# Kernel tuning notes

Hardware: AMD Instinct MI355X
Metric: run time of the kernel (lower is better)

## Reference

```python
import jax, jax.numpy as jnp
import numpy as np

EMBED = 1024
HEADS = 16
HEAD_DIM = EMBED // HEADS
MASKED_BIAS = -10000.0


def setup_inputs() -> dict:
    key = jax.random.key(0)
    k1, k2, k3 = jax.random.split(key, 3)
    hidden_states = jax.random.normal(k1, (4, 2048, EMBED), dtype=jnp.float32)
    c_attn_w = jax.random.normal(k2, (EMBED, 3 * EMBED), dtype=jnp.float32) * 0.02
    c_attn_b = jnp.zeros((3 * EMBED,), dtype=jnp.float32)
    c_proj_w = jax.random.normal(k3, (EMBED, EMBED), dtype=jnp.float32) * 0.02
    c_proj_b = jnp.zeros((EMBED,), dtype=jnp.float32)
    return {
        "hidden_states": hidden_states,
        "c_attn_w": c_attn_w,
        "c_attn_b": c_attn_b,
        "c_proj_w": c_proj_w,
        "c_proj_b": c_proj_b,
    }


def reference(hidden_states, c_attn_w, c_attn_b, c_proj_w, c_proj_b):
    B, S, E = hidden_states.shape
    # QKV projection (Conv1D == x @ W + b)
    qkv = hidden_states @ c_attn_w + c_attn_b  # [B,S,3E]
    q, k, v = jnp.split(qkv, 3, axis=-1)
    def split_heads(t):
        return t.reshape(B, S, HEADS, HEAD_DIM).transpose(0, 2, 1, 3)  # [B,H,S,D]
    q, k, v = split_heads(q), split_heads(k), split_heads(v)
    # scaled attention scores
    scores = jnp.einsum("bhqd,bhkd->bhqk", q, k) / jnp.float32(HEAD_DIM) ** 0.5
    causal = jnp.tril(jnp.ones((S, S), dtype=bool))
    scores = jnp.where(causal[None, None], scores, jnp.float32(MASKED_BIAS))
    attn_weights = jax.nn.softmax(scores, axis=-1)
    attn_out = jnp.einsum("bhqk,bhkd->bhqd", attn_weights, v)
    attn_out = attn_out.transpose(0, 2, 1, 3).reshape(B, S, E)
    out = attn_out @ c_proj_w + c_proj_b
    return out
```

## Files before the change

kernel.cpp:

```cpp
#include <hip/hip_runtime.h>
#include <hip/hip_bf16.h>

#define EMB 1024
#define SEQ 2048
#define ATT_SCALE 0.18033688011112042f

typedef __bf16 bf16x8 __attribute__((ext_vector_type(8)));
typedef float f32x4 __attribute__((ext_vector_type(4)));
typedef float f32x16 __attribute__((ext_vector_type(16)));

__device__ __forceinline__ unsigned short f2bf(float f) {
    union { float f; unsigned int u; } v; v.f = f;
    unsigned int r = (v.u + 0x7FFFu + ((v.u >> 16) & 1u)) >> 16;
    return (unsigned short)r;
}

__device__ __forceinline__ void async_load16(const void* g, void* l) {
    __builtin_amdgcn_global_load_lds(
        (const __attribute__((address_space(1))) unsigned int*)g,
        (__attribute__((address_space(3))) unsigned int*)l, 16, 0, 0);
}

__global__ void cvt_bf16(const float4* __restrict__ in, ushort4* __restrict__ out, int n4) {
    int i = blockIdx.x * blockDim.x + threadIdx.x;
    int stride = gridDim.x * blockDim.x;
    for (; i < n4; i += stride) {
        float4 v = in[i];
        ushort4 o;
        o.x = f2bf(v.x); o.y = f2bf(v.y); o.z = f2bf(v.z); o.w = f2bf(v.w);
        out[i] = o;
    }
}

__global__ void transpose_cvt(const float* __restrict__ in, unsigned short* __restrict__ out,
                              int R, int C) {
    __shared__ float tile[32][33];
    int bx = blockIdx.x * 32;
    int by = blockIdx.y * 32;
    int tx = threadIdx.x & 31;
    int ty = threadIdx.x >> 5;
    #pragma unroll
    for (int i = 0; i < 32; i += 8)
        tile[ty + i][tx] = in[(size_t)(by + ty + i) * C + bx + tx];
    __syncthreads();
    #pragma unroll
    for (int i = 0; i < 32; i += 8)
        out[(size_t)(bx + ty + i) * R + by + tx] = f2bf(tile[tx][ty + i]);
}

#define BM 128
#define BN 128
#define BK 64

template<bool OUT_BF16, bool FUSE_VT, int NPER>
__global__ __launch_bounds__(256, 2)
void gemm_bf16(const unsigned short* __restrict__ A,
               const unsigned short* __restrict__ Bt,
               const float* __restrict__ bias,
               void* __restrict__ Cout,
               unsigned short* __restrict__ Vtout,
               int M, int N, int K) {
    __shared__ unsigned short As[BM * 64];
    __shared__ unsigned short Bs[BN * 64];
    const int tid = threadIdx.x;
    const int id = blockIdx.x;
    const int xcd = id & 7;
    const int loc = id >> 3;
    const int m0 = (loc / NPER) * BM;
    const int n0 = (xcd * NPER + (loc % NPER)) * BN;
    const int lane = tid & 63;
    const int wave = tid >> 6;
    const int wm = (wave & 1) * 64;
    const int wn = (wave >> 1) * 64;
    const int l31 = lane & 31;
    const int half = lane >> 5;
    const int r8 = lane >> 3;
    const int pc = lane & 7;

    f32x16 acc[2][2] = {};

    for (int k0 = 0; k0 < K; k0 += BK) {
        __syncthreads();
        #pragma unroll
        for (int i = 0; i < 4; i++) {
            int r = wave * 32 + i * 8 + r8;
            int lc = pc ^ (r & 7);
            async_load16(&A[(size_t)(m0 + r) * K + k0 + lc * 8], &As[(wave * 32 + i * 8) * 64]);
            async_load16(&Bt[(size_t)(n0 + r) * K + k0 + lc * 8], &Bs[(wave * 32 + i * 8) * 64]);
        }
        __syncthreads();
        #pragma unroll
        for (int ks = 0; ks < 4; ks++) {
            const int lch = ks * 2 + half;
            bf16x8 af[2], bf[2];
            #pragma unroll
            for (int t = 0; t < 2; t++) {
                int ra = wm + t * 32 + l31;
                int rb = wn + t * 32 + l31;
                af[t] = *(const bf16x8*)&As[ra * 64 + (lch ^ (ra & 7)) * 8];
                bf[t] = *(const bf16x8*)&Bs[rb * 64 + (lch ^ (rb & 7)) * 8];
            }
            #pragma unroll
            for (int mt = 0; mt < 2; mt++)
                #pragma unroll
                for (int nt = 0; nt < 2; nt++)
                    acc[mt][nt] = __builtin_amdgcn_mfma_f32_32x32x16_bf16(
                        af[mt], bf[nt], acc[mt][nt], 0, 0, 0);
        }
    }
    #pragma unroll
    for (int mt = 0; mt < 2; mt++) {
        #pragma unroll
        for (int nt = 0; nt < 2; nt++) {
            int col = n0 + wn + nt * 32 + l31;
            float bv = bias[col];
            if (FUSE_VT && col >= 2 * EMB) {
                int dd = col - 2 * EMB;
                #pragma unroll
                for (int g = 0; g < 4; g++) {
                    int row0 = m0 + wm + mt * 32 + 8 * g + 4 * half;
                    int b = row0 >> 11;
                    int s = row0 & 2047;
                    ushort4 o;
                    o.x = f2bf(acc[mt][nt][4 * g + 0] + bv);
                    o.y = f2bf(acc[mt][nt][4 * g + 1] + bv);
                    o.z = f2bf(acc[mt][nt][4 * g + 2] + bv);
                    o.w = f2bf(acc[mt][nt][4 * g + 3] + bv);
                    *(ushort4*)&Vtout[((size_t)(b * 16) * 64 + dd) * SEQ + s] = o;
                }
            } else {
                #pragma unroll
                for (int reg = 0; reg < 16; reg++) {
                    int row = m0 + wm + mt * 32 + (reg & 3) + 8 * (reg >> 2) + 4 * half;
                    float val = acc[mt][nt][reg] + bv;
                    if (OUT_BF16)
                        ((unsigned short*)Cout)[(size_t)row * N + col] = f2bf(val);
                    else
                        ((float*)Cout)[(size_t)row * N + col] = val;
                }
            }
        }
    }
}

__global__ __launch_bounds__(256, 4)
void attention(const unsigned short* __restrict__ qkv,
               const unsigned short* __restrict__ vt,
               unsigned short* __restrict__ outb) {
    __shared__ unsigned short smem[2 * 2 * 64 * 64];
    const int tid = threadIdx.x;
    const int lane = tid & 63;
    const int wave = tid >> 6;
    const int l31 = lane & 31;
    const int half = lane >> 5;

    const int id = blockIdx.x;
    const int m4 = ((id >> 8) << 2) | (id & 3);
    const int qt = (int)((0xF12C4A97865B3DE0ULL >> (m4 * 4)) & 15);
    const int bh = (id & 255) >> 2;
    const int b = bh >> 4;
    const int h = bh & 15;

    const int qs = qt * 128 + wave * 32 + l31;
    const size_t qgrow = (size_t)b * SEQ + qs;

    bf16x8 qf[4];
    #pragma unroll
    for (int dt = 0; dt < 4; dt++)
        qf[dt] = *(const bf16x8*)&qkv[qgrow * 3072 + h * 64 + dt * 16 + half * 8];

    f32x16 o[2] = {};
    float lsum = 0.f;

    const int nkb = 2 * qt + 2;
    const int qmax_w = qt * 128 + wave * 32 + 31;

    const int row8 = lane >> 3;
    const int chsw = ((lane & 7) ^ row8) * 8;

    #pragma unroll
    for (int i = 0; i < 2; i++) {
        int row = wave * 16 + i * 8 + row8;
        async_load16(&qkv[(size_t)(b * SEQ + row) * 3072 + EMB + h * 64 + chsw],
                     &smem[(wave * 16 + i * 8) * 64]);
        async_load16(&vt[(size_t)(bh * 64 + row) * SEQ + chsw],
                     &smem[4096 + (wave * 16 + i * 8) * 64]);
    }

    for (int kb = 0; kb < nkb; kb++) {
        unsigned short* Ks = smem + (kb & 1) * 8192;
        unsigned short* Vs = Ks + 4096;
        __syncthreads();
        if (kb + 1 < nkb) {
            unsigned short* nb = smem + ((kb + 1) & 1) * 8192;
            #pragma unroll
            for (int i = 0; i < 2; i++) {
                int row = wave * 16 + i * 8 + row8;
                async_load16(&qkv[(size_t)(b * SEQ + (kb + 1) * 64 + row) * 3072 + EMB + h * 64 + chsw],
                             &nb[(wave * 16 + i * 8) * 64]);
                async_load16(&vt[(size_t)(bh * 64 + row) * SEQ + (kb + 1) * 64 + chsw],
                             &nb[4096 + (wave * 16 + i * 8) * 64]);
            }
        }
        if (kb * 64 > qmax_w) continue;

        f32x16 st[2] = {};
        __builtin_amdgcn_s_setprio(1);
        #pragma unroll
        for (int dt = 0; dt < 4; dt++) {
            #pragma unroll
            for (int ct = 0; ct < 2; ct++) {
                int kr = ct * 32 + l31;
                bf16x8 kf = *(const bf16x8*)&Ks[kr * 64 + ((dt * 2 + half) ^ (l31 & 7)) * 8];
                st[ct] = __builtin_amdgcn_mfma_f32_32x32x16_bf16(kf, qf[dt], st[ct], 0, 0, 0);
            }
        }
        __builtin_amdgcn_s_setprio(0);

        if (kb * 64 + 63 > qt * 128 + wave * 32) {
            #pragma unroll
            for (int ct = 0; ct < 2; ct++)
                #pragma unroll
                for (int r = 0; r < 16; r++) {
                    int cg = kb * 64 + ct * 32 + (r & 3) + 8 * (r >> 2) + 4 * half;
                    if (cg > qs) st[ct][r] = -1e9f;
                }
        }

        #pragma unroll
        for (int r = 0; r < 16; r++) {
            st[0][r] = exp2f(st[0][r] * ATT_SCALE);
            st[1][r] = exp2f(st[1][r] * ATT_SCALE);
        }
        float ts[8];
        #pragma unroll
        for (int r = 0; r < 8; r++)
            ts[r] = (st[0][r] + st[1][r]) + (st[0][r + 8] + st[1][r + 8]);
        #pragma unroll
        for (int s = 4; s > 0; s >>= 1)
            #pragma unroll
            for (int r = 0; r < s; r++) ts[r] += ts[r + s];
        lsum += ts[0];

        unsigned int pk[2][8];
        #pragma unroll
        for (int t = 0; t < 2; t++)
            #pragma unroll
            for (int i = 0; i < 8; i++) {
                __hip_bfloat162 pb = __float22bfloat162_rn(float2{st[t][2 * i], st[t][2 * i + 1]});
                union { __hip_bfloat162 b; unsigned int u; } cv; cv.b = pb;
                pk[t][i] = cv.u;
            }

        __builtin_amdgcn_s_setprio(1);
        #pragma unroll
        for (int kt = 0; kt < 4; kt++) {
            const int t = kt >> 1, e = kt & 1;
            unsigned int a0 = pk[t][4 * e + 0], b0 = pk[t][4 * e + 2];
            unsigned int a1 = pk[t][4 * e + 1], b1 = pk[t][4 * e + 3];
            asm("v_permlane32_swap_b32 %0, %1" : "+v"(a0), "+v"(b0));
            asm("v_permlane32_swap_b32 %0, %1" : "+v"(a1), "+v"(b1));
            union { uint4 u; bf16x8 v; } pf;
            pf.u.x = a0; pf.u.y = a1; pf.u.z = b0; pf.u.w = b1;
            #pragma unroll
            for (int dt = 0; dt < 2; dt++) {
                int vr = dt * 32 + l31;
                bf16x8 vf = *(const bf16x8*)&Vs[vr * 64 + ((kt * 2 + half) ^ (l31 & 7)) * 8];
                o[dt] = __builtin_amdgcn_mfma_f32_32x32x16_bf16(vf, pf.v, o[dt], 0, 0, 0);
            }
        }
        __builtin_amdgcn_s_setprio(0);
    }

    __syncthreads();
    float lt = lsum + __shfl_xor(lsum, 32, 64);
    float inv = 1.0f / lt;
    #pragma unroll
    for (int dt = 0; dt < 2; dt++)
        #pragma unroll
        for (int r = 0; r < 16; r++) {
            int d = dt * 32 + (r & 3) + 8 * (r >> 2) + 4 * half;
            smem[(wave * 32 + l31) * 72 + d] = f2bf(o[dt][r] * inv);
        }
    __syncthreads();
    #pragma unroll
    for (int i = 0; i < 4; i++) {
        int c = tid + 256 * i;
        int row = c >> 3;
        int ch = (c & 7) * 8;
        uint4 v = *(const uint4*)&smem[row * 72 + ch];
        *(uint4*)&outb[(size_t)(b * SEQ + qt * 128 + row) * EMB + h * 64 + ch] = v;
    }
}

extern "C" void kernel_launch(void* const* d_in, const int* in_sizes, int n_in,
                              void* d_out, int out_size, void* d_ws, size_t ws_size,
                              hipStream_t stream) {
    const float* X     = (const float*)d_in[0];
    const float* Wqkv  = (const float*)d_in[1];
    const float* bqkv  = (const float*)d_in[2];
    const float* Wproj = (const float*)d_in[3];
    const float* bproj = (const float*)d_in[4];
    float* out = (float*)d_out;

    char* ws = (char*)d_ws;
    unsigned short* Xb     = (unsigned short*)(ws);
    unsigned short* WqkvT  = (unsigned short*)(ws + 16777216);
    unsigned short* WprojT = (unsigned short*)(ws + 23068672);
    unsigned short* qkvb   = (unsigned short*)(ws + 25165824);
    unsigned short* Vt     = (unsigned short*)(ws + 75497472);
    unsigned short* attnb  = (unsigned short*)(ws + 92274688);

    cvt_bf16<<<2048, 256, 0, stream>>>((const float4*)X, (ushort4*)Xb, (4 * 2048 * 1024) / 4);
    transpose_cvt<<<dim3(3072 / 32, 1024 / 32), 256, 0, stream>>>(Wqkv, WqkvT, 1024, 3072);
    transpose_cvt<<<dim3(1024 / 32, 1024 / 32), 256, 0, stream>>>(Wproj, WprojT, 1024, 1024);
    gemm_bf16<true, true, 3><<<(3072 / BN) * (8192 / BM), 256, 0, stream>>>(
        Xb, WqkvT, bqkv, qkvb, Vt, 8192, 3072, 1024);
    attention<<<1024, 256, 0, stream>>>(qkvb, Vt, attnb);
    gemm_bf16<false, false, 1><<<(1024 / BN) * (8192 / BM), 256, 0, stream>>>(
        attnb, WprojT, bproj, out, nullptr, 8192, 1024, 1024);
}
```

Baseline: 267.6 us.

## Pair causal query tiles per attention block with triple-buffered K/V pipeline

Each attention block now handles two query tiles (p and 15-p) in sequence, so every block processes the same number of K/V tiles (34) and the causal triangle no longer leaves blocks imbalanced. The grid halves to 512 blocks. The K/V staging moves from double to triple buffering with explicit vmcnt waits and raw barriers, giving loads more lead time. LDS use grows and launch bounds drop to 2 blocks per CU, which lowers occupancy.

```diff
diff --git a/kernel.cpp b/kernel.cpp
--- a/kernel.cpp
+++ b/kernel.cpp
@@ -143,11 +143,11 @@
     }
 }
 
-__global__ __launch_bounds__(256, 4)
+__global__ __launch_bounds__(256, 2)
 void attention(const unsigned short* __restrict__ qkv,
                const unsigned short* __restrict__ vt,
                unsigned short* __restrict__ outb) {
-    __shared__ unsigned short smem[2 * 2 * 64 * 64];
+    __shared__ unsigned short smem[3 * 2 * 64 * 64 + 128 * 72];
     const int tid = threadIdx.x;
     const int lane = tid & 63;
     const int wave = tid >> 6;
@@ -155,142 +155,170 @@
     const int half = lane >> 5;
 
     const int id = blockIdx.x;
-    const int m4 = ((id >> 8) << 2) | (id & 3);
-    const int qt = (int)((0xF12C4A97865B3DE0ULL >> (m4 * 4)) & 15);
-    const int bh = (id & 255) >> 2;
+    const int bh = id & 63;
+    const int p = id >> 6;
     const int b = bh >> 4;
     const int h = bh & 15;
-
-    const int qs = qt * 128 + wave * 32 + l31;
-    const size_t qgrow = (size_t)b * SEQ + qs;
+    const int qt_hi = 15 - p;
+    const int qt_lo = p;
+    const int nkb_hi = 2 * qt_hi + 2;
+    const int NT = 34;
+
+    const int row8 = lane >> 3;
+    const int chsw = ((lane & 7) ^ row8) * 8;
+
+    auto stage = [&](int t) {
+        unsigned short* dst = smem + (t % 3) * 8192;
+        int kv0 = (t < nkb_hi) ? t * 64 : (t - nkb_hi) * 64;
+        #pragma unroll
+        for (int i = 0; i < 2; i++) {
+            int row = wave * 16 + i * 8 + row8;
+            async_load16(&qkv[(size_t)(b * SEQ + kv0 + row) * 3072 + EMB + h * 64 + chsw],
+                         &dst[(wave * 16 + i * 8) * 64]);
+            async_load16(&vt[(size_t)(bh * 64 + row) * SEQ + kv0 + chsw],
+                         &dst[4096 + (wave * 16 + i * 8) * 64]);
+        }
+    };
 
     bf16x8 qf[4];
-    #pragma unroll
-    for (int dt = 0; dt < 4; dt++)
-        qf[dt] = *(const bf16x8*)&qkv[qgrow * 3072 + h * 64 + dt * 16 + half * 8];
+    auto loadQ = [&](int qtq) {
+        size_t qrow = (size_t)b * SEQ + qtq * 128 + wave * 32 + l31;
+        #pragma unroll
+        for (int dt = 0; dt < 4; dt++)
+            qf[dt] = *(const bf16x8*)&qkv[qrow * 3072 + h * 64 + dt * 16 + half * 8];
+    };
 
     f32x16 o[2] = {};
     float lsum = 0.f;
 
-    const int nkb = 2 * qt + 2;
-    const int qmax_w = qt * 128 + wave * 32 + 31;
-
-    const int row8 = lane >> 3;
-    const int chsw = ((lane & 7) ^ row8) * 8;
-
-    #pragma unroll
-    for (int i = 0; i < 2; i++) {
-        int row = wave * 16 + i * 8 + row8;
-        async_load16(&qkv[(size_t)(b * SEQ + row) * 3072 + EMB + h * 64 + chsw],
-                     &smem[(wave * 16 + i * 8) * 64]);
-        async_load16(&vt[(size_t)(bh * 64 + row) * SEQ + chsw],
-                     &smem[4096 + (wave * 16 + i * 8) * 64]);
+    auto write_out = [&](int qtw) {
+        unsigned short* eb = smem + 24576;
+        float lt = lsum + __shfl_xor(lsum, 32, 64);
+        float inv = 1.0f / lt;
+        #pragma unroll
+        for (int dt = 0; dt < 2; dt++)
+            #pragma unroll
+            for (int r = 0; r < 16; r++) {
+                int d = dt * 32 + (r & 3) + 8 * (r >> 2) + 4 * half;
+                eb[(wave * 32 + l31) * 72 + d] = f2bf(o[dt][r] * inv);
+            }
+        asm volatile("s_waitcnt lgkmcnt(0)" ::: "memory");
+        __builtin_amdgcn_s_barrier();
+        __builtin_amdgcn_sched_barrier(0);
+        #pragma unroll
+        for (int i = 0; i < 4; i++) {
+            int c = tid + 256 * i;
+            int row = c >> 3;
+            int ch = (c & 7) * 8;
+            uint4 v = *(const uint4*)&eb[row * 72 + ch];
+            *(uint4*)&outb[(size_t)(b * SEQ + qtw * 128 + row) * EMB + h * 64 + ch] = v;
+        }
+    };
+
+    stage(0);
+    stage(1);
+    loadQ(qt_hi);
+
+    int qt = qt_hi;
+    int qs = qt_hi * 128 + wave * 32 + l31;
+    int kb0 = 0;
+
+    for (int t = 0; t < NT; t++) {
+        if (t + 1 < NT) asm volatile("s_waitcnt vmcnt(4)" ::: "memory");
+        else            asm volatile("s_waitcnt vmcnt(0)" ::: "memory");
+        __builtin_amdgcn_s_barrier();
+        __builtin_amdgcn_sched_barrier(0);
+        if (t + 2 < NT) stage(t + 2);
+
+        unsigned short* Ks = smem + (t % 3) * 8192;
+        unsigned short* Vs = Ks + 4096;
+        const int kb = t - kb0;
+        const int qmax_w = qt * 128 + wave * 32 + 31;
+
+        if (kb * 64 <= qmax_w) {
+            f32x16 st[2] = {};
+            __builtin_amdgcn_s_setprio(1);
+            #pragma unroll
+            for (int dt = 0; dt < 4; dt++) {
+                #pragma unroll
+                for (int ct = 0; ct < 2; ct++) {
+                    int kr = ct * 32 + l31;
+                    bf16x8 kf = *(const bf16x8*)&Ks[kr * 64 + ((dt * 2 + half) ^ (l31 & 7)) * 8];
+                    st[ct] = __builtin_amdgcn_mfma_f32_32x32x16_bf16(kf, qf[dt], st[ct], 0, 0, 0);
+                }
+            }
+            __builtin_amdgcn_s_setprio(0);
+
+            if (kb * 64 + 63 > qt * 128 + wave * 32) {
+                #pragma unroll
+                for (int ct = 0; ct < 2; ct++)
+                    #pragma unroll
+                    for (int r = 0; r < 16; r++) {
+                        int cg = kb * 64 + ct * 32 + (r & 3) + 8 * (r >> 2) + 4 * half;
+                        if (cg > qs) st[ct][r] = -1e9f;
+                    }
+            }
+
+            #pragma unroll
+            for (int r = 0; r < 16; r++) {
+                st[0][r] = exp2f(st[0][r] * ATT_SCALE);
+                st[1][r] = exp2f(st[1][r] * ATT_SCALE);
+            }
+            float ts[8];
+            #pragma unroll
+            for (int r = 0; r < 8; r++)
+                ts[r] = (st[0][r] + st[1][r]) + (st[0][r + 8] + st[1][r + 8]);
+            #pragma unroll
+            for (int s = 4; s > 0; s >>= 1)
+                #pragma unroll
+                for (int r = 0; r < s; r++) ts[r] += ts[r + s];
+            lsum += ts[0];
+
+            unsigned int pk[2][8];
+            #pragma unroll
+            for (int tt = 0; tt < 2; tt++)
+                #pragma unroll
+                for (int i = 0; i < 8; i++) {
+                    __hip_bfloat162 pb = __float22bfloat162_rn(float2{st[tt][2 * i], st[tt][2 * i + 1]});
+                    union { __hip_bfloat162 b; unsigned int u; } cv; cv.b = pb;
+                    pk[tt][i] = cv.u;
+                }
+
+            __builtin_amdgcn_s_setprio(1);
+            #pragma unroll
+            for (int kt = 0; kt < 4; kt++) {
+                const int tt = kt >> 1, e = kt & 1;
+                unsigned int a0 = pk[tt][4 * e + 0], b0 = pk[tt][4 * e + 2];
+                unsigned int a1 = pk[tt][4 * e + 1], b1 = pk[tt][4 * e + 3];
+                asm("v_permlane32_swap_b32 %0, %1" : "+v"(a0), "+v"(b0));
+                asm("v_permlane32_swap_b32 %0, %1" : "+v"(a1), "+v"(b1));
+                union { uint4 u; bf16x8 v; } pf;
+                pf.u.x = a0; pf.u.y = a1; pf.u.z = b0; pf.u.w = b1;
+                #pragma unroll
+                for (int dt = 0; dt < 2; dt++) {
+                    int vr = dt * 32 + l31;
+                    bf16x8 vf = *(const bf16x8*)&Vs[vr * 64 + ((kt * 2 + half) ^ (l31 & 7)) * 8];
+                    o[dt] = __builtin_amdgcn_mfma_f32_32x32x16_bf16(vf, pf.v, o[dt], 0, 0, 0);
+                }
+            }
+            __builtin_amdgcn_s_setprio(0);
+        }
+
+        if (t == nkb_hi - 1) {
+            write_out(qt_hi);
+            #pragma unroll
+            for (int dt = 0; dt < 2; dt++)
+                #pragma unroll
+                for (int r = 0; r < 16; r++) o[dt][r] = 0.f;
+            lsum = 0.f;
+            qt = qt_lo;
+            qs = qt_lo * 128 + wave * 32 + l31;
+            kb0 = nkb_hi;
+            loadQ(qt_lo);
+        }
     }
 
-    for (int kb = 0; kb < nkb; kb++) {
-        unsigned short* Ks = smem + (kb & 1) * 8192;
-        unsigned short* Vs = Ks + 4096;
-        __syncthreads();
-        if (kb + 1 < nkb) {
-            unsigned short* nb = smem + ((kb + 1) & 1) * 8192;
-            #pragma unroll
-            for (int i = 0; i < 2; i++) {
-                int row = wave * 16 + i * 8 + row8;
-                async_load16(&qkv[(size_t)(b * SEQ + (kb + 1) * 64 + row) * 3072 + EMB + h * 64 + chsw],
-                             &nb[(wave * 16 + i * 8) * 64]);
-                async_load16(&vt[(size_t)(bh * 64 + row) * SEQ + (kb + 1) * 64 + chsw],
-                             &nb[4096 + (wave * 16 + i * 8) * 64]);
-            }
-        }
-        if (kb * 64 > qmax_w) continue;
-
-        f32x16 st[2] = {};
-        __builtin_amdgcn_s_setprio(1);
-        #pragma unroll
-        for (int dt = 0; dt < 4; dt++) {
-            #pragma unroll
-            for (int ct = 0; ct < 2; ct++) {
-                int kr = ct * 32 + l31;
-                bf16x8 kf = *(const bf16x8*)&Ks[kr * 64 + ((dt * 2 + half) ^ (l31 & 7)) * 8];
-                st[ct] = __builtin_amdgcn_mfma_f32_32x32x16_bf16(kf, qf[dt], st[ct], 0, 0, 0);
-            }
-        }
-        __builtin_amdgcn_s_setprio(0);
-
-        if (kb * 64 + 63 > qt * 128 + wave * 32) {
-            #pragma unroll
-            for (int ct = 0; ct < 2; ct++)
-                #pragma unroll
-                for (int r = 0; r < 16; r++) {
-                    int cg = kb * 64 + ct * 32 + (r & 3) + 8 * (r >> 2) + 4 * half;
-                    if (cg > qs) st[ct][r] = -1e9f;
-                }
-        }
-
-        #pragma unroll
-        for (int r = 0; r < 16; r++) {
-            st[0][r] = exp2f(st[0][r] * ATT_SCALE);
-            st[1][r] = exp2f(st[1][r] * ATT_SCALE);
-        }
-        float ts[8];
-        #pragma unroll
-        for (int r = 0; r < 8; r++)
-            ts[r] = (st[0][r] + st[1][r]) + (st[0][r + 8] + st[1][r + 8]);
-        #pragma unroll
-        for (int s = 4; s > 0; s >>= 1)
-            #pragma unroll
-            for (int r = 0; r < s; r++) ts[r] += ts[r + s];
-        lsum += ts[0];
-
-        unsigned int pk[2][8];
-        #pragma unroll
-        for (int t = 0; t < 2; t++)
-            #pragma unroll
-            for (int i = 0; i < 8; i++) {
-                __hip_bfloat162 pb = __float22bfloat162_rn(float2{st[t][2 * i], st[t][2 * i + 1]});
-                union { __hip_bfloat162 b; unsigned int u; } cv; cv.b = pb;
-                pk[t][i] = cv.u;
-            }
-
-        __builtin_amdgcn_s_setprio(1);
-        #pragma unroll
-        for (int kt = 0; kt < 4; kt++) {
-            const int t = kt >> 1, e = kt & 1;
-            unsigned int a0 = pk[t][4 * e + 0], b0 = pk[t][4 * e + 2];
-            unsigned int a1 = pk[t][4 * e + 1], b1 = pk[t][4 * e + 3];
-            asm("v_permlane32_swap_b32 %0, %1" : "+v"(a0), "+v"(b0));
-            asm("v_permlane32_swap_b32 %0, %1" : "+v"(a1), "+v"(b1));
-            union { uint4 u; bf16x8 v; } pf;
-            pf.u.x = a0; pf.u.y = a1; pf.u.z = b0; pf.u.w = b1;
-            #pragma unroll
-            for (int dt = 0; dt < 2; dt++) {
-                int vr = dt * 32 + l31;
-                bf16x8 vf = *(const bf16x8*)&Vs[vr * 64 + ((kt * 2 + half) ^ (l31 & 7)) * 8];
-                o[dt] = __builtin_amdgcn_mfma_f32_32x32x16_bf16(vf, pf.v, o[dt], 0, 0, 0);
-            }
-        }
-        __builtin_amdgcn_s_setprio(0);
-    }
-
-    __syncthreads();
-    float lt = lsum + __shfl_xor(lsum, 32, 64);
-    float inv = 1.0f / lt;
-    #pragma unroll
-    for (int dt = 0; dt < 2; dt++)
-        #pragma unroll
-        for (int r = 0; r < 16; r++) {
-            int d = dt * 32 + (r & 3) + 8 * (r >> 2) + 4 * half;
-            smem[(wave * 32 + l31) * 72 + d] = f2bf(o[dt][r] * inv);
-        }
-    __syncthreads();
-    #pragma unroll
-    for (int i = 0; i < 4; i++) {
-        int c = tid + 256 * i;
-        int row = c >> 3;
-        int ch = (c & 7) * 8;
-        uint4 v = *(const uint4*)&smem[row * 72 + ch];
-        *(uint4*)&outb[(size_t)(b * SEQ + qt * 128 + row) * EMB + h * 64 + ch] = v;
-    }
+    write_out(qt_lo);
 }
 
 extern "C" void kernel_launch(void* const* d_in, const int* in_sizes, int n_in,
@@ -316,7 +344,7 @@
     transpose_cvt<<<dim3(1024 / 32, 1024 / 32), 256, 0, stream>>>(Wproj, WprojT, 1024, 1024);
     gemm_bf16<true, true, 3><<<(3072 / BN) * (8192 / BM), 256, 0, stream>>>(
         Xb, WqkvT, bqkv, qkvb, Vt, 8192, 3072, 1024);
-    attention<<<1024, 256, 0, stream>>>(qkvb, Vt, attnb);
+    attention<<<512, 256, 0, stream>>>(qkvb, Vt, attnb);
     gemm_bf16<false, false, 1><<<(1024 / BN) * (8192 / BM), 256, 0, stream>>>(
         attnb, WprojT, bproj, out, nullptr, 8192, 1024, 1024);
 }
```

Measured after the change: 261.3 us. -2.4%, faster.

## Unroll attention K/V double-buffer loop with explicit waits and remap block indices

Applied to the files above, without the earlier changes.

Restructures the attention kernel's K/V pipeline into a two-stage unrolled loop over separate LDS buffers. Each stage issues the next tile's async loads before computing the current one, then waits on vmcnt and uses raw s_barrier with sched_barrier fences. The block-index mapping is changed so consecutive blocks cover different heads for better L2 locality. The epilogue now writes 8-byte ushort4 stores straight from registers instead of staging through LDS. The loop removes the per-tile early skip of fully masked tiles, and the direct stores are less coalesced than the previous 16-byte staged writes.

```diff
diff --git a/kernel.cpp b/kernel.cpp
--- a/kernel.cpp
+++ b/kernel.cpp
@@ -147,7 +147,8 @@
 void attention(const unsigned short* __restrict__ qkv,
                const unsigned short* __restrict__ vt,
                unsigned short* __restrict__ outb) {
-    __shared__ unsigned short smem[2 * 2 * 64 * 64];
+    __shared__ unsigned short bufA[2 * 64 * 64];
+    __shared__ unsigned short bufB[2 * 64 * 64];
     const int tid = threadIdx.x;
     const int lane = tid & 63;
     const int wave = tid >> 6;
@@ -155,55 +156,44 @@
     const int half = lane >> 5;
 
     const int id = blockIdx.x;
-    const int m4 = ((id >> 8) << 2) | (id & 3);
+    const int c = id & 7;
+    const int g = id >> 3;
+    const int m4 = ((g >> 5) << 2) | (g & 3);
     const int qt = (int)((0xF12C4A97865B3DE0ULL >> (m4 * 4)) & 15);
-    const int bh = (id & 255) >> 2;
+    const int bh = (((g >> 2) & 7) << 3) | c;
     const int b = bh >> 4;
     const int h = bh & 15;
 
     const int qs = qt * 128 + wave * 32 + l31;
-    const size_t qgrow = (size_t)b * SEQ + qs;
+    const int nkb = 2 * qt + 2;
+    const int qmax_w = qt * 128 + wave * 32 + 31;
+
+    const int row8 = lane >> 3;
+    const int chsw = ((lane & 7) ^ row8) * 8;
 
     bf16x8 qf[4];
-    #pragma unroll
-    for (int dt = 0; dt < 4; dt++)
-        qf[dt] = *(const bf16x8*)&qkv[qgrow * 3072 + h * 64 + dt * 16 + half * 8];
+    {
+        size_t qrow = (size_t)b * SEQ + qs;
+        #pragma unroll
+        for (int dt = 0; dt < 4; dt++)
+            qf[dt] = *(const bf16x8*)&qkv[qrow * 3072 + h * 64 + dt * 16 + half * 8];
+    }
+
+    auto stage = [&](unsigned short* dst, int kb) {
+        #pragma unroll
+        for (int i = 0; i < 2; i++) {
+            int row = wave * 16 + i * 8 + row8;
+            async_load16(&qkv[(size_t)(b * SEQ + kb * 64 + row) * 3072 + EMB + h * 64 + chsw],
+                         &dst[(wave * 16 + i * 8) * 64]);
+            async_load16(&vt[(size_t)(bh * 64 + row) * SEQ + kb * 64 + chsw],
+                         &dst[4096 + (wave * 16 + i * 8) * 64]);
+        }
+    };
 
     f32x16 o[2] = {};
     float lsum = 0.f;
 
-    const int nkb = 2 * qt + 2;
-    const int qmax_w = qt * 128 + wave * 32 + 31;
-
-    const int row8 = lane >> 3;
-    const int chsw = ((lane & 7) ^ row8) * 8;
-
-    #pragma unroll
-    for (int i = 0; i < 2; i++) {
-        int row = wave * 16 + i * 8 + row8;
-        async_load16(&qkv[(size_t)(b * SEQ + row) * 3072 + EMB + h * 64 + chsw],
-                     &smem[(wave * 16 + i * 8) * 64]);
-        async_load16(&vt[(size_t)(bh * 64 + row) * SEQ + chsw],
-                     &smem[4096 + (wave * 16 + i * 8) * 64]);
-    }
-
-    for (int kb = 0; kb < nkb; kb++) {
-        unsigned short* Ks = smem + (kb & 1) * 8192;
-        unsigned short* Vs = Ks + 4096;
-        __syncthreads();
-        if (kb + 1 < nkb) {
-            unsigned short* nb = smem + ((kb + 1) & 1) * 8192;
-            #pragma unroll
-            for (int i = 0; i < 2; i++) {
-                int row = wave * 16 + i * 8 + row8;
-                async_load16(&qkv[(size_t)(b * SEQ + (kb + 1) * 64 + row) * 3072 + EMB + h * 64 + chsw],
-                             &nb[(wave * 16 + i * 8) * 64]);
-                async_load16(&vt[(size_t)(bh * 64 + row) * SEQ + (kb + 1) * 64 + chsw],
-                             &nb[4096 + (wave * 16 + i * 8) * 64]);
-            }
-        }
-        if (kb * 64 > qmax_w) continue;
-
+    auto compute = [&](const unsigned short* Ks, const unsigned short* Vs, int kb) {
         f32x16 st[2] = {};
         __builtin_amdgcn_s_setprio(1);
         #pragma unroll
@@ -244,20 +234,20 @@
 
         unsigned int pk[2][8];
         #pragma unroll
-        for (int t = 0; t < 2; t++)
+        for (int tt = 0; tt < 2; tt++)
             #pragma unroll
             for (int i = 0; i < 8; i++) {
-                __hip_bfloat162 pb = __float22bfloat162_rn(float2{st[t][2 * i], st[t][2 * i + 1]});
+                __hip_bfloat162 pb = __float22bfloat162_rn(float2{st[tt][2 * i], st[tt][2 * i + 1]});
                 union { __hip_bfloat162 b; unsigned int u; } cv; cv.b = pb;
-                pk[t][i] = cv.u;
+                pk[tt][i] = cv.u;
             }
 
         __builtin_amdgcn_s_setprio(1);
         #pragma unroll
         for (int kt = 0; kt < 4; kt++) {
-            const int t = kt >> 1, e = kt & 1;
-            unsigned int a0 = pk[t][4 * e + 0], b0 = pk[t][4 * e + 2];
-            unsigned int a1 = pk[t][4 * e + 1], b1 = pk[t][4 * e + 3];
+            const int tt = kt >> 1, e = kt & 1;
+            unsigned int a0 = pk[tt][4 * e + 0], b0 = pk[tt][4 * e + 2];
+            unsigned int a1 = pk[tt][4 * e + 1], b1 = pk[tt][4 * e + 3];
             asm("v_permlane32_swap_b32 %0, %1" : "+v"(a0), "+v"(b0));
             asm("v_permlane32_swap_b32 %0, %1" : "+v"(a1), "+v"(b1));
             union { uint4 u; bf16x8 v; } pf;
@@ -270,26 +260,41 @@
             }
         }
         __builtin_amdgcn_s_setprio(0);
-    }
-
-    __syncthreads();
+    };
+
+    stage(bufA, 0);
+    asm volatile("s_waitcnt vmcnt(0)" ::: "memory");
+    __builtin_amdgcn_s_barrier();
+    __builtin_amdgcn_sched_barrier(0);
+
+    const int nit = nkb >> 1;
+    for (int i = 0; i < nit; i++) {
+        stage(bufB, 2 * i + 1);
+        compute(bufA, bufA + 4096, 2 * i);
+        asm volatile("s_waitcnt vmcnt(0)" ::: "memory");
+        __builtin_amdgcn_s_barrier();
+        __builtin_amdgcn_sched_barrier(0);
+        if (i + 1 < nit) stage(bufA, 2 * i + 2);
+        compute(bufB, bufB + 4096, 2 * i + 1);
+        asm volatile("s_waitcnt vmcnt(0)" ::: "memory");
+        __builtin_amdgcn_s_barrier();
+        __builtin_amdgcn_sched_barrier(0);
+    }
+
     float lt = lsum + __shfl_xor(lsum, 32, 64);
     float inv = 1.0f / lt;
     #pragma unroll
-    for (int dt = 0; dt < 2; dt++)
-        #pragma unroll
-        for (int r = 0; r < 16; r++) {
-            int d = dt * 32 + (r & 3) + 8 * (r >> 2) + 4 * half;
-            smem[(wave * 32 + l31) * 72 + d] = f2bf(o[dt][r] * inv);
-        }
-    __syncthreads();
-    #pragma unroll
-    for (int i = 0; i < 4; i++) {
-        int c = tid + 256 * i;
-        int row = c >> 3;
-        int ch = (c & 7) * 8;
-        uint4 v = *(const uint4*)&smem[row * 72 + ch];
-        *(uint4*)&outb[(size_t)(b * SEQ + qt * 128 + row) * EMB + h * 64 + ch] = v;
+    for (int dt = 0; dt < 2; dt++) {
+        #pragma unroll
+        for (int gq = 0; gq < 4; gq++) {
+            ushort4 ov;
+            ov.x = f2bf(o[dt][4 * gq + 0] * inv);
+            ov.y = f2bf(o[dt][4 * gq + 1] * inv);
+            ov.z = f2bf(o[dt][4 * gq + 2] * inv);
+            ov.w = f2bf(o[dt][4 * gq + 3] * inv);
+            int d0 = h * 64 + dt * 32 + 8 * gq + 4 * half;
+            *(ushort4*)&outb[(size_t)(b * SEQ + qs) * EMB + d0] = ov;
+        }
     }
 }
 
```

Measured after the change: 315.3 us. +17.8%, slower.
